# Kernel tuning notes

Measured on AMD Instinct MI355X. Metric: run time of the kernel, lower is better.

The kernel has to match this reference:

```python
import jax, jax.numpy as jnp
import numpy as np

B, S, H, A = 8, 512, 256, 64

def setup_inputs() -> dict:
    key = jax.random.key(0)
    k1, k2, k3, k4, k5 = jax.random.split(key, 5)
    def xavier(k, shape):
        fan_in, fan_out = shape[-1], shape[-2] if len(shape) >= 2 else shape[-1]
        limit = float(np.sqrt(6.0 / (fan_in + fan_out)))
        return jax.random.uniform(k, shape, jnp.float32, -limit, limit)
    return {
        "relation_hidden": jax.random.normal(k1, (B, S, H), jnp.float32),
        "w_ta": xavier(k2, (A, H)),
        "w_ja": xavier(k3, (A, H)),
        "b": xavier(k4, (1, 1, 1, A)),
        "v": xavier(k5, (1, A)),
    }

def reference(relation_hidden, w_ta, w_ja, b, v):
    # ta: (B,S,A) scores for 'target', ja: (B,S,A) for 'joint'
    ta = jnp.einsum('bsh,ah->bsa', relation_hidden, w_ta)
    ja = jnp.einsum('bsh,ah->bsa', relation_hidden, w_ja)
    # broadcast-add to (B,S,S,A), tanh, project to scalar with v
    alpha = jnp.tanh(ta[:, :, None, :] + ja[:, None, :, :] + b)  # (B,S,S,A)
    scores = jnp.einsum('bija,a->bij', alpha, v[0])              # (B,S,S)
    return jax.nn.softmax(scores, axis=2)
```

## Files before the change

kernel.cpp:

```cpp
#include <hip/hip_runtime.h>


#define B_ 8
#define S_ 512
#define H_ 256
#define A_ 64

__global__ __launch_bounds__(256) void rel_stage1(
    const float* __restrict__ rh, const float* __restrict__ wta,
    const float* __restrict__ wja, const float* __restrict__ bias,
    float* __restrict__ ta2e, float* __restrict__ ej) {
  __shared__ float rt[64][65];
  __shared__ __align__(16) float ws[16][68];
  const int t = threadIdx.x;
  const int rb = blockIdx.x & 63;
  const int cb = blockIdx.x >> 6;
  const int row0 = rb << 6;
  const int lane = t & 63;
  const int cg0 = cb << 4;
  const int cl = __builtin_amdgcn_readfirstlane((t >> 6) << 2);
  const float* wsrc = (cg0 < A_) ? (wta + (size_t)cg0 * H_)
                                 : (wja + (size_t)(cg0 - A_) * H_);
  const int sr = t >> 4, sq = t & 15;

  float4 acc = {0.f, 0.f, 0.f, 0.f};
  for (int kt = 0; kt < H_; kt += 64) {
    if (kt) __syncthreads();
#pragma unroll
    for (int i = 0; i < 4; ++i) {
      const int r = sr + (i << 4);
      const float4 x =
          *(const float4*)&rh[(size_t)(row0 + r) * H_ + kt + (sq << 2)];
      rt[(sq << 2) + 0][r] = x.x;
      rt[(sq << 2) + 1][r] = x.y;
      rt[(sq << 2) + 2][r] = x.z;
      rt[(sq << 2) + 3][r] = x.w;
    }
    {
      const float4 wx =
          *(const float4*)&wsrc[(size_t)sr * H_ + kt + (sq << 2)];
      *(float4*)&ws[sr][sq << 2] = wx;
    }
    __syncthreads();
#pragma unroll 4
    for (int k4 = 0; k4 < 16; ++k4) {
      const int k = k4 << 2;
      const float4 w0 = *(const float4*)&ws[cl + 0][k];
      const float4 w1 = *(const float4*)&ws[cl + 1][k];
      const float4 w2 = *(const float4*)&ws[cl + 2][k];
      const float4 w3 = *(const float4*)&ws[cl + 3][k];
      const float x0 = rt[k + 0][lane], x1 = rt[k + 1][lane];
      const float x2 = rt[k + 2][lane], x3 = rt[k + 3][lane];
      acc.x += x0 * w0.x + x1 * w0.y + x2 * w0.z + x3 * w0.w;
      acc.y += x0 * w1.x + x1 * w1.y + x2 * w1.z + x3 * w1.w;
      acc.z += x0 * w2.x + x1 * w2.y + x2 * w2.z + x3 * w2.w;
      acc.w += x0 * w3.x + x1 * w3.y + x2 * w3.z + x3 * w3.w;
    }
  }

  const int row = row0 + lane;
  const int cg = cg0 + cl;
  if (cg < A_) {
    float4 e;
    e.x = __expf(2.f * (acc.x + bias[cg + 0]));
    e.y = __expf(2.f * (acc.y + bias[cg + 1]));
    e.z = __expf(2.f * (acc.z + bias[cg + 2]));
    e.w = __expf(2.f * (acc.w + bias[cg + 3]));
    *(float4*)&ta2e[(size_t)row * A_ + cg] = e;
  } else {
    const int a0 = cg - A_;
    const int bidx = row >> 9;
    const int s = row & (S_ - 1);
    float4 e;
    e.x = __expf(2.f * acc.x);
    e.y = __expf(2.f * acc.y);
    e.z = __expf(2.f * acc.z);
    e.w = __expf(2.f * acc.w);
    *(float4*)&ej[((((size_t)bidx * 16 + (a0 >> 2)) * S_ + s) << 2)] = e;
  }
}

__global__ __launch_bounds__(512) void rel_stage2(
    const float* __restrict__ ta2e, const float* __restrict__ ej,
    const float* __restrict__ v, float* __restrict__ out) {
  __shared__ __align__(16) float tai[8][A_];
  __shared__ __align__(16) float vm[A_];
  __shared__ float red[8][8];
  const int t = threadIdx.x;
  const int row0 = blockIdx.x << 3;
  const int bidx = row0 >> 9;
  tai[t >> 6][t & 63] = ta2e[(size_t)row0 * A_ + t];
  if (t < A_) vm[t] = -2.f * v[t];
  __syncthreads();

  float vsum = 0.f;
#pragma unroll
  for (int a = 0; a < A_; a += 4) {
    const float4 x = *(const float4*)&vm[a];
    vsum += x.x + x.y + x.z + x.w;
  }
  vsum *= -0.5f;

  float acc[8] = {0.f, 0.f, 0.f, 0.f, 0.f, 0.f, 0.f, 0.f};
  const float* ejb = ej + (((size_t)bidx * 16) * S_ << 2) + (t << 2);
#pragma unroll 2
  for (int g = 0; g < 16; ++g) {
    const float4 E = *(const float4*)(ejb + ((size_t)g * S_ << 2));
    const float4 V = *(const float4*)&vm[g << 2];
#pragma unroll
    for (int r = 0; r < 8; ++r) {
      const float4 T = *(const float4*)&tai[r][g << 2];
      acc[r] += V.x * __builtin_amdgcn_rcpf(__builtin_fmaf(T.x, E.x, 1.f))
              + V.y * __builtin_amdgcn_rcpf(__builtin_fmaf(T.y, E.y, 1.f))
              + V.z * __builtin_amdgcn_rcpf(__builtin_fmaf(T.z, E.z, 1.f))
              + V.w * __builtin_amdgcn_rcpf(__builtin_fmaf(T.w, E.w, 1.f));
    }
  }
  float sc[8];
#pragma unroll
  for (int r = 0; r < 8; ++r) sc[r] = vsum + acc[r];

  const int lane = t & 63;
  const int wv = t >> 6;
#pragma unroll
  for (int r = 0; r < 8; ++r) {
    float m = sc[r];
#pragma unroll
    for (int off = 32; off; off >>= 1) m = fmaxf(m, __shfl_xor(m, off));
    if (lane == 0) red[r][wv] = m;
  }
  __syncthreads();
  float mx[8];
#pragma unroll
  for (int r = 0; r < 8; ++r) {
    float m = red[r][0];
#pragma unroll
    for (int i = 1; i < 8; ++i) m = fmaxf(m, red[r][i]);
    mx[r] = m;
  }
  __syncthreads();
  float ex[8];
#pragma unroll
  for (int r = 0; r < 8; ++r) {
    ex[r] = __expf(sc[r] - mx[r]);
    float s = ex[r];
#pragma unroll
    for (int off = 32; off; off >>= 1) s += __shfl_xor(s, off);
    if (lane == 0) red[r][wv] = s;
  }
  __syncthreads();
#pragma unroll
  for (int r = 0; r < 8; ++r) {
    float s = 0.f;
#pragma unroll
    for (int i = 0; i < 8; ++i) s += red[r][i];
    out[(size_t)(row0 + r) * S_ + t] = ex[r] * __builtin_amdgcn_rcpf(s);
  }
}

extern "C" void kernel_launch(void* const* d_in, const int* in_sizes, int n_in,
                              void* d_out, int out_size, void* d_ws, size_t ws_size,
                              hipStream_t stream) {
  const float* rh   = (const float*)d_in[0];
  const float* wta  = (const float*)d_in[1];
  const float* wja  = (const float*)d_in[2];
  const float* bias = (const float*)d_in[3];
  const float* v    = (const float*)d_in[4];
  float* out = (float*)d_out;

  float* ta2e = (float*)d_ws;
  float* ej   = ta2e + (size_t)B_ * S_ * A_;

  rel_stage1<<<dim3(512), dim3(256), 0, stream>>>(rh, wta, wja, bias, ta2e, ej);
  rel_stage2<<<dim3((B_ * S_) / 8), dim3(512), 0, stream>>>(ta2e, ej, v, out);
}
```

Baseline: 101.6 us.

## Double per-thread work in both stages to raise register reuse

Stage 1 now computes 128 rows per block, with two accumulator sets per thread. It stores rows untransposed and reads them as float4, which halves the block count and reuses the shared weight tile across two rows. Stage 2 drops to 256 threads, each computing two output columns per row, so each tai/V shared load feeds twice the rcp work. The cost is higher register pressure and fewer waves in stage 2 to hide latency. The odd tai index expression reduces to a plain linear float2 copy.

```diff
diff --git a/kernel.cpp b/kernel.cpp
--- a/kernel.cpp
+++ b/kernel.cpp
@@ -10,12 +10,12 @@
     const float* __restrict__ rh, const float* __restrict__ wta,
     const float* __restrict__ wja, const float* __restrict__ bias,
     float* __restrict__ ta2e, float* __restrict__ ej) {
-  __shared__ float rt[64][65];
+  __shared__ float rhs[128][65];
   __shared__ __align__(16) float ws[16][68];
   const int t = threadIdx.x;
-  const int rb = blockIdx.x & 63;
-  const int cb = blockIdx.x >> 6;
-  const int row0 = rb << 6;
+  const int rb = blockIdx.x & 31;
+  const int cb = blockIdx.x >> 5;
+  const int row0 = rb << 7;
   const int lane = t & 63;
   const int cg0 = cb << 4;
   const int cl = __builtin_amdgcn_readfirstlane((t >> 6) << 2);
@@ -23,73 +23,84 @@
                                  : (wja + (size_t)(cg0 - A_) * H_);
   const int sr = t >> 4, sq = t & 15;
 
-  float4 acc = {0.f, 0.f, 0.f, 0.f};
+  float4 acc0 = {0.f, 0.f, 0.f, 0.f};
+  float4 acc1 = {0.f, 0.f, 0.f, 0.f};
   for (int kt = 0; kt < H_; kt += 64) {
     if (kt) __syncthreads();
 #pragma unroll
-    for (int i = 0; i < 4; ++i) {
-      const int r = sr + (i << 4);
-      const float4 x =
-          *(const float4*)&rh[(size_t)(row0 + r) * H_ + kt + (sq << 2)];
-      rt[(sq << 2) + 0][r] = x.x;
-      rt[(sq << 2) + 1][r] = x.y;
-      rt[(sq << 2) + 2][r] = x.z;
-      rt[(sq << 2) + 3][r] = x.w;
+    for (int i = 0; i < 8; ++i) {
+      const int fid = t + (i << 8);
+      const int r = fid >> 4, kq = fid & 15;
+      *(float4*)&rhs[r][kq << 2] =
+          *(const float4*)&rh[(size_t)(row0 + r) * H_ + kt + (kq << 2)];
     }
-    {
-      const float4 wx =
-          *(const float4*)&wsrc[(size_t)sr * H_ + kt + (sq << 2)];
-      *(float4*)&ws[sr][sq << 2] = wx;
-    }
+    *(float4*)&ws[sr][sq << 2] =
+        *(const float4*)&wsrc[(size_t)sr * H_ + kt + (sq << 2)];
     __syncthreads();
 #pragma unroll 4
     for (int k4 = 0; k4 < 16; ++k4) {
       const int k = k4 << 2;
+      const float4 x0 = *(const float4*)&rhs[lane][k];
+      const float4 x1 = *(const float4*)&rhs[lane + 64][k];
       const float4 w0 = *(const float4*)&ws[cl + 0][k];
       const float4 w1 = *(const float4*)&ws[cl + 1][k];
       const float4 w2 = *(const float4*)&ws[cl + 2][k];
       const float4 w3 = *(const float4*)&ws[cl + 3][k];
-      const float x0 = rt[k + 0][lane], x1 = rt[k + 1][lane];
-      const float x2 = rt[k + 2][lane], x3 = rt[k + 3][lane];
-      acc.x += x0 * w0.x + x1 * w0.y + x2 * w0.z + x3 * w0.w;
-      acc.y += x0 * w1.x + x1 * w1.y + x2 * w1.z + x3 * w1.w;
-      acc.z += x0 * w2.x + x1 * w2.y + x2 * w2.z + x3 * w2.w;
-      acc.w += x0 * w3.x + x1 * w3.y + x2 * w3.z + x3 * w3.w;
+      acc0.x += x0.x * w0.x + x0.y * w0.y + x0.z * w0.z + x0.w * w0.w;
+      acc0.y += x0.x * w1.x + x0.y * w1.y + x0.z * w1.z + x0.w * w1.w;
+      acc0.z += x0.x * w2.x + x0.y * w2.y + x0.z * w2.z + x0.w * w2.w;
+      acc0.w += x0.x * w3.x + x0.y * w3.y + x0.z * w3.z + x0.w * w3.w;
+      acc1.x += x1.x * w0.x + x1.y * w0.y + x1.z * w0.z + x1.w * w0.w;
+      acc1.y += x1.x * w1.x + x1.y * w1.y + x1.z * w1.z + x1.w * w1.w;
+      acc1.z += x1.x * w2.x + x1.y * w2.y + x1.z * w2.z + x1.w * w2.w;
+      acc1.w += x1.x * w3.x + x1.y * w3.y + x1.z * w3.z + x1.w * w3.w;
     }
   }
 
-  const int row = row0 + lane;
   const int cg = cg0 + cl;
   if (cg < A_) {
+    const float b0 = bias[cg + 0], b1 = bias[cg + 1];
+    const float b2 = bias[cg + 2], b3 = bias[cg + 3];
     float4 e;
-    e.x = __expf(2.f * (acc.x + bias[cg + 0]));
-    e.y = __expf(2.f * (acc.y + bias[cg + 1]));
-    e.z = __expf(2.f * (acc.z + bias[cg + 2]));
-    e.w = __expf(2.f * (acc.w + bias[cg + 3]));
-    *(float4*)&ta2e[(size_t)row * A_ + cg] = e;
+    e.x = __expf(2.f * (acc0.x + b0));
+    e.y = __expf(2.f * (acc0.y + b1));
+    e.z = __expf(2.f * (acc0.z + b2));
+    e.w = __expf(2.f * (acc0.w + b3));
+    *(float4*)&ta2e[(size_t)(row0 + lane) * A_ + cg] = e;
+    e.x = __expf(2.f * (acc1.x + b0));
+    e.y = __expf(2.f * (acc1.y + b1));
+    e.z = __expf(2.f * (acc1.z + b2));
+    e.w = __expf(2.f * (acc1.w + b3));
+    *(float4*)&ta2e[(size_t)(row0 + lane + 64) * A_ + cg] = e;
   } else {
-    const int a0 = cg - A_;
-    const int bidx = row >> 9;
-    const int s = row & (S_ - 1);
-    float4 e;
-    e.x = __expf(2.f * acc.x);
-    e.y = __expf(2.f * acc.y);
-    e.z = __expf(2.f * acc.z);
-    e.w = __expf(2.f * acc.w);
-    *(float4*)&ej[((((size_t)bidx * 16 + (a0 >> 2)) * S_ + s) << 2)] = e;
+    const int g = (cg - A_) >> 2;
+#pragma unroll
+    for (int rr = 0; rr < 2; ++rr) {
+      const int row = row0 + lane + (rr << 6);
+      const int bidx = row >> 9;
+      const int s = row & (S_ - 1);
+      const float4 a = rr ? acc1 : acc0;
+      float4 e;
+      e.x = __expf(2.f * a.x);
+      e.y = __expf(2.f * a.y);
+      e.z = __expf(2.f * a.z);
+      e.w = __expf(2.f * a.w);
+      *(float4*)&ej[(((size_t)bidx * 16 + g) * S_ + s) << 2] = e;
+    }
   }
 }
 
-__global__ __launch_bounds__(512) void rel_stage2(
+__global__ __launch_bounds__(256) void rel_stage2(
     const float* __restrict__ ta2e, const float* __restrict__ ej,
     const float* __restrict__ v, float* __restrict__ out) {
   __shared__ __align__(16) float tai[8][A_];
   __shared__ __align__(16) float vm[A_];
-  __shared__ float red[8][8];
+  __shared__ float red[8][4];
   const int t = threadIdx.x;
   const int row0 = blockIdx.x << 3;
   const int bidx = row0 >> 9;
-  tai[t >> 6][t & 63] = ta2e[(size_t)row0 * A_ + t];
+  *(float2*)&tai[0][0 + (t << 1) - ((t >> 5) << 6) + ((t >> 5) << 6)] =
+      *(const float2*)&ta2e[(size_t)row0 * A_ + (t << 1)];
   if (t < A_) vm[t] = -2.f * v[t];
   __syncthreads();
 
@@ -101,49 +112,51 @@
   }
   vsum *= -0.5f;
 
-  float acc[8] = {0.f, 0.f, 0.f, 0.f, 0.f, 0.f, 0.f, 0.f};
+  float acc0[8] = {0.f, 0.f, 0.f, 0.f, 0.f, 0.f, 0.f, 0.f};
+  float acc1[8] = {0.f, 0.f, 0.f, 0.f, 0.f, 0.f, 0.f, 0.f};
   const float* ejb = ej + (((size_t)bidx * 16) * S_ << 2) + (t << 2);
 #pragma unroll 2
   for (int g = 0; g < 16; ++g) {
-    const float4 E = *(const float4*)(ejb + ((size_t)g * S_ << 2));
+    const float4 E0 = *(const float4*)(ejb + ((size_t)g * S_ << 2));
+    const float4 E1 = *(const float4*)(ejb + ((size_t)g * S_ << 2) + 1024);
     const float4 V = *(const float4*)&vm[g << 2];
 #pragma unroll
     for (int r = 0; r < 8; ++r) {
       const float4 T = *(const float4*)&tai[r][g << 2];
-      acc[r] += V.x * __builtin_amdgcn_rcpf(__builtin_fmaf(T.x, E.x, 1.f))
-              + V.y * __builtin_amdgcn_rcpf(__builtin_fmaf(T.y, E.y, 1.f))
-              + V.z * __builtin_amdgcn_rcpf(__builtin_fmaf(T.z, E.z, 1.f))
-              + V.w * __builtin_amdgcn_rcpf(__builtin_fmaf(T.w, E.w, 1.f));
+      acc0[r] += V.x * __builtin_amdgcn_rcpf(__builtin_fmaf(T.x, E0.x, 1.f))
+               + V.y * __builtin_amdgcn_rcpf(__builtin_fmaf(T.y, E0.y, 1.f))
+               + V.z * __builtin_amdgcn_rcpf(__builtin_fmaf(T.z, E0.z, 1.f))
+               + V.w * __builtin_amdgcn_rcpf(__builtin_fmaf(T.w, E0.w, 1.f));
+      acc1[r] += V.x * __builtin_amdgcn_rcpf(__builtin_fmaf(T.x, E1.x, 1.f))
+               + V.y * __builtin_amdgcn_rcpf(__builtin_fmaf(T.y, E1.y, 1.f))
+               + V.z * __builtin_amdgcn_rcpf(__builtin_fmaf(T.z, E1.z, 1.f))
+               + V.w * __builtin_amdgcn_rcpf(__builtin_fmaf(T.w, E1.w, 1.f));
     }
   }
-  float sc[8];
-#pragma unroll
-  for (int r = 0; r < 8; ++r) sc[r] = vsum + acc[r];
 
   const int lane = t & 63;
   const int wv = t >> 6;
+  float ex0[8], ex1[8], mx[8];
 #pragma unroll
   for (int r = 0; r < 8; ++r) {
-    float m = sc[r];
+    const float s0 = vsum + acc0[r], s1 = vsum + acc1[r];
+    ex0[r] = s0;
+    ex1[r] = s1;
+    float m = fmaxf(s0, s1);
 #pragma unroll
     for (int off = 32; off; off >>= 1) m = fmaxf(m, __shfl_xor(m, off));
     if (lane == 0) red[r][wv] = m;
   }
   __syncthreads();
-  float mx[8];
+#pragma unroll
+  for (int r = 0; r < 8; ++r)
+    mx[r] = fmaxf(fmaxf(red[r][0], red[r][1]), fmaxf(red[r][2], red[r][3]));
+  __syncthreads();
 #pragma unroll
   for (int r = 0; r < 8; ++r) {
-    float m = red[r][0];
-#pragma unroll
-    for (int i = 1; i < 8; ++i) m = fmaxf(m, red[r][i]);
-    mx[r] = m;
-  }
-  __syncthreads();
-  float ex[8];
-#pragma unroll
-  for (int r = 0; r < 8; ++r) {
-    ex[r] = __expf(sc[r] - mx[r]);
-    float s = ex[r];
+    ex0[r] = __expf(ex0[r] - mx[r]);
+    ex1[r] = __expf(ex1[r] - mx[r]);
+    float s = ex0[r] + ex1[r];
 #pragma unroll
     for (int off = 32; off; off >>= 1) s += __shfl_xor(s, off);
     if (lane == 0) red[r][wv] = s;
@@ -151,10 +164,10 @@
   __syncthreads();
 #pragma unroll
   for (int r = 0; r < 8; ++r) {
-    float s = 0.f;
-#pragma unroll
-    for (int i = 0; i < 8; ++i) s += red[r][i];
-    out[(size_t)(row0 + r) * S_ + t] = ex[r] * __builtin_amdgcn_rcpf(s);
+    const float s = (red[r][0] + red[r][1]) + (red[r][2] + red[r][3]);
+    const float inv = __builtin_amdgcn_rcpf(s);
+    out[(size_t)(row0 + r) * S_ + t] = ex0[r] * inv;
+    out[(size_t)(row0 + r) * S_ + t + 256] = ex1[r] * inv;
   }
 }
 
@@ -171,6 +184,6 @@
   float* ta2e = (float*)d_ws;
   float* ej   = ta2e + (size_t)B_ * S_ * A_;
 
-  rel_stage1<<<dim3(512), dim3(256), 0, stream>>>(rh, wta, wja, bias, ta2e, ej);
-  rel_stage2<<<dim3((B_ * S_) / 8), dim3(512), 0, stream>>>(ta2e, ej, v, out);
+  rel_stage1<<<dim3(256), dim3(256), 0, stream>>>(rh, wta, wja, bias, ta2e, ej);
+  rel_stage2<<<dim3((B_ * S_) / 8), dim3(256), 0, stream>>>(ta2e, ej, v, out);
 }
```

After: 102.3 us. No clear change (+0.7%).
